# Kernel optimization log

Measured on AMD Instinct MI355X. Metric: run time of the kernel, lower is better.

Reference implementation:

```python
import jax, jax.numpy as jnp
import numpy as np

N = 50000      # nodes
E = 400000     # edges
IN_DIM = 128
HID = 64
HEADS1 = 4
OUT_DIM = 64
NEG_SLOPE = 0.2


def _gat_layer(x, W, attn_l, attn_r, bias, src, dst, heads, out_feats):
    # x: [N, F_in]; W: [F_in, heads*out]; attn_l/attn_r: [heads, out]; bias: [heads*out]
    n = x.shape[0]
    feat = (x @ W).reshape(n, heads, out_feats)              # [N, H, D]
    el = jnp.sum(feat * attn_l, axis=-1)                     # [N, H]
    er = jnp.sum(feat * attn_r, axis=-1)                     # [N, H]
    e = jax.nn.leaky_relu(el[src] + er[dst], NEG_SLOPE)      # [E, H]
    # segment softmax over incoming edges per destination node
    emax = jax.ops.segment_max(e, dst, num_segments=n)       # [N, H]
    ex = jnp.exp(e - emax[dst])                              # [E, H]
    denom = jax.ops.segment_sum(ex, dst, num_segments=n)     # [N, H]
    alpha = ex / denom[dst]                                  # [E, H]
    msg = alpha[:, :, None] * feat[src]                      # [E, H, D]
    rst = jax.ops.segment_sum(msg, dst, num_segments=n)      # [N, H, D]
    return rst + bias.reshape(1, heads, out_feats)


def setup_inputs() -> dict:
    key = jax.random.key(0)
    ks = jax.random.split(key, 12)
    features = jax.random.normal(ks[0], (N, IN_DIM), dtype=jnp.float32)
    src = jax.random.randint(ks[1], (E,), 0, N, dtype=jnp.int32)
    dst = jax.random.randint(ks[2], (E,), 0, N, dtype=jnp.int32)
    s1 = 1.0 / np.sqrt(IN_DIM)
    s2 = 1.0 / np.sqrt(HEADS1 * HID)
    W1 = jax.random.normal(ks[3], (IN_DIM, HEADS1 * HID), dtype=jnp.float32) * s1
    attn_l1 = jax.random.normal(ks[4], (HEADS1, HID), dtype=jnp.float32) * 0.1
    attn_r1 = jax.random.normal(ks[5], (HEADS1, HID), dtype=jnp.float32) * 0.1
    b1 = jnp.zeros((HEADS1 * HID,), dtype=jnp.float32)
    W2 = jax.random.normal(ks[6], (HEADS1 * HID, OUT_DIM), dtype=jnp.float32) * s2
    attn_l2 = jax.random.normal(ks[7], (1, OUT_DIM), dtype=jnp.float32) * 0.1
    attn_r2 = jax.random.normal(ks[8], (1, OUT_DIM), dtype=jnp.float32) * 0.1
    b2 = jnp.zeros((OUT_DIM,), dtype=jnp.float32)
    return {"features": features, "src": src, "dst": dst,
            "W1": W1, "attn_l1": attn_l1, "attn_r1": attn_r1, "b1": b1,
            "W2": W2, "attn_l2": attn_l2, "attn_r2": attn_r2, "b2": b2}


def reference(features, src, dst, W1, attn_l1, attn_r1, b1, W2, attn_l2, attn_r2, b2):
    h = _gat_layer(features, W1, attn_l1, attn_r1, b1, src, dst, HEADS1, HID)  # [N, 4, 64]
    h = h.reshape(h.shape[0], -1)                                             # flatten heads
    h = _gat_layer(h, W2, attn_l2, attn_r2, b2, src, dst, 1, OUT_DIM)         # [N, 1, 64]
    return h
```

## Files before the change

### kernel.cpp

```cpp
#include <hip/hip_runtime.h>
#include <hip/hip_bf16.h>

#define N_NODES 50000
#define N_EDGES 400000
#define IN_DIM 128
#define HID 64
#define HEADS 4
#define L1_OUT (HEADS * HID)
#define OUT_DIM 64
#define NEG_SLOPE 0.2f
#define SCAN_B 256
#define DCHUNK 128
#define HIST_B 1563

typedef short bf16x8 __attribute__((ext_vector_type(8)));
typedef float f32x4 __attribute__((ext_vector_type(4)));

__device__ __forceinline__ float leaky(float x) { return x > 0.f ? x : NEG_SLOPE * x; }

__device__ __forceinline__ unsigned short bfh(float x) {
    unsigned u = __float_as_uint(x);
    return (unsigned short)((u + 0x7fffu + ((u >> 16) & 1u)) >> 16);
}
__device__ __forceinline__ float fb(unsigned short h) {
    return __uint_as_float(((unsigned)h) << 16);
}

__global__ void hist_wprep_kernel(const int* __restrict__ dst, int* __restrict__ cnt,
                                  const float* __restrict__ W1, const float* __restrict__ W2,
                                  unsigned short* __restrict__ W1fh, unsigned short* __restrict__ W1fl,
                                  unsigned short* __restrict__ W2fh, unsigned short* __restrict__ W2fl) {
    int bid = blockIdx.x;
    if (bid < HIST_B) {
        int e = bid * 256 + threadIdx.x;
        if (e < N_EDGES) atomicAdd(&cnt[dst[e]], 1);
        return;
    }
    int s = (bid - HIST_B) * 256 + threadIdx.x;
    if (s < 4096) {
        int lane = s & 63, ks = (s >> 6) & 3, ntile = s >> 8;
        int n = ntile * 16 + (lane & 15);
        int kb = ks * 32 + (lane >> 4) * 8;
#pragma unroll
        for (int j = 0; j < 8; ++j) {
            float w = W1[(kb + j) * L1_OUT + n];
            unsigned short h = bfh(w);
            W1fh[s * 8 + j] = h;
            W1fl[s * 8 + j] = bfh(w - fb(h));
        }
    } else if (s < 6144) {
        int s2 = s - 4096;
        int lane = s2 & 63, ks = (s2 >> 6) & 7, ntile = s2 >> 9;
        int n = ntile * 16 + (lane & 15);
        int kb = ks * 32 + (lane >> 4) * 8;
#pragma unroll
        for (int j = 0; j < 8; ++j) {
            float w = W2[(kb + j) * OUT_DIM + n];
            unsigned short h = bfh(w);
            W2fh[s2 * 8 + j] = h;
            W2fl[s2 * 8 + j] = bfh(w - fb(h));
        }
    }
}

__global__ void scanA_kernel(const int* __restrict__ cnt, int* __restrict__ texcl,
                             int* __restrict__ bsum) {
    __shared__ int sh[SCAN_B];
    int tid = threadIdx.x;
    int i = blockIdx.x * SCAN_B + tid;
    int v = (i < N_NODES) ? cnt[i] : 0;
    sh[tid] = v;
    __syncthreads();
    for (int off = 1; off < SCAN_B; off <<= 1) {
        int t = (tid >= off) ? sh[tid - off] : 0;
        __syncthreads();
        sh[tid] += t;
        __syncthreads();
    }
    if (i < N_NODES) texcl[i] = sh[tid] - v;
    if (tid == SCAN_B - 1) bsum[blockIdx.x] = sh[tid];
}

__global__ void scanB_kernel(const int* __restrict__ bsum, int* __restrict__ bexcl, int nb) {
    __shared__ int sh[SCAN_B];
    int tid = threadIdx.x;
    int v = (tid < nb) ? bsum[tid] : 0;
    sh[tid] = v;
    __syncthreads();
    for (int off = 1; off < SCAN_B; off <<= 1) {
        int t = (tid >= off) ? sh[tid - off] : 0;
        __syncthreads();
        sh[tid] += t;
        __syncthreads();
    }
    if (tid < nb) bexcl[tid] = sh[tid] - v;
}

__global__ void scanC_kernel(const int* __restrict__ texcl, const int* __restrict__ bexcl,
                             int* __restrict__ row) {
    int i = blockIdx.x * blockDim.x + threadIdx.x;
    if (i < N_NODES) row[i] = texcl[i] + bexcl[i >> 8];
    if (blockIdx.x == 0 && threadIdx.x == 0) row[N_NODES] = N_EDGES;
}

__global__ void fill_kernel(const int* __restrict__ src, const int* __restrict__ dst,
                            const int* __restrict__ row, int* __restrict__ fc,
                            int* __restrict__ perm_src) {
    int e = blockIdx.x * blockDim.x + threadIdx.x;
    if (e >= N_EDGES) return;
    int d = dst[e];
    int p = row[d] + atomicAdd(&fc[d], 1);
    perm_src[p] = src[e];
}

__global__ __launch_bounds__(512) void gemm1_kernel(const float* __restrict__ X,
                                                    const unsigned short* __restrict__ W1fh,
                                                    const unsigned short* __restrict__ W1fl,
                                                    const float* __restrict__ al1,
                                                    const float* __restrict__ ar1,
                                                    unsigned short* __restrict__ feat1b,
                                                    float* __restrict__ el1,
                                                    float* __restrict__ er1) {
    __shared__ unsigned short Ah[4 * 4 * 64 * 8];
    __shared__ unsigned short Al[4 * 4 * 64 * 8];
    int t = threadIdx.x;
    int m0 = blockIdx.x * 64;

    {
        int m = t >> 3;
        int k0 = (t & 7) * 16;
        int mfrag = m >> 4, mrow = m & 15;
        bool valid = (m0 + m) < N_NODES;
        const float4* xr = (const float4*)&X[(size_t)(m0 + m) * IN_DIM];
#pragma unroll
        for (int g = 0; g < 4; ++g) {
            int k = k0 + g * 4;
            float4 v = valid ? xr[k >> 2] : float4{0.f, 0.f, 0.f, 0.f};
            int kstep = k >> 5, kk = k & 31;
            int lane = mrow + 16 * (kk >> 3);
            int j0 = kk & 7;
            int base = ((mfrag * 4 + kstep) * 64 + lane) * 8 + j0;
            unsigned short h0 = bfh(v.x), h1 = bfh(v.y), h2 = bfh(v.z), h3 = bfh(v.w);
            *(ushort4*)&Ah[base] = make_ushort4(h0, h1, h2, h3);
            *(ushort4*)&Al[base] = make_ushort4(bfh(v.x - fb(h0)), bfh(v.y - fb(h1)),
                                                bfh(v.z - fb(h2)), bfh(v.w - fb(h3)));
        }
    }
    __syncthreads();

    int w = t >> 6, lane = t & 63;
    int wr = w >> 2, wc = w & 3;
    f32x4 acc[2][4];
#pragma unroll
    for (int mi = 0; mi < 2; ++mi)
#pragma unroll
        for (int nf = 0; nf < 4; ++nf) acc[mi][nf] = f32x4{0.f, 0.f, 0.f, 0.f};

#pragma unroll
    for (int kstep = 0; kstep < 4; ++kstep) {
        bf16x8 a_h[2], a_l[2];
#pragma unroll
        for (int mi = 0; mi < 2; ++mi) {
            int slot = (((wr * 2 + mi) * 4 + kstep) * 64 + lane) * 8;
            a_h[mi] = *(const bf16x8*)&Ah[slot];
            a_l[mi] = *(const bf16x8*)&Al[slot];
        }
#pragma unroll
        for (int nf = 0; nf < 4; ++nf) {
            int slot = (((wc * 4 + nf) * 4 + kstep) * 64 + lane) * 8;
            bf16x8 b_h = *(const bf16x8*)&W1fh[slot];
            bf16x8 b_l = *(const bf16x8*)&W1fl[slot];
#pragma unroll
            for (int mi = 0; mi < 2; ++mi) {
                acc[mi][nf] = __builtin_amdgcn_mfma_f32_16x16x32_bf16(a_h[mi], b_h, acc[mi][nf], 0, 0, 0);
                acc[mi][nf] = __builtin_amdgcn_mfma_f32_16x16x32_bf16(a_h[mi], b_l, acc[mi][nf], 0, 0, 0);
                acc[mi][nf] = __builtin_amdgcn_mfma_f32_16x16x32_bf16(a_l[mi], b_h, acc[mi][nf], 0, 0, 0);
            }
        }
    }

    int fq = lane >> 4, fr = lane & 15;
#pragma unroll
    for (int mi = 0; mi < 2; ++mi) {
#pragma unroll
        for (int j = 0; j < 4; ++j) {
            int r = m0 + wr * 32 + mi * 16 + fq * 4 + j;
            if (r >= N_NODES) continue;
#pragma unroll
            for (int nf = 0; nf < 4; ++nf) {
                int c = wc * 64 + nf * 16 + fr;
                feat1b[(size_t)r * L1_OUT + c] = bfh(acc[mi][nf][j]);
            }
        }
    }

    float al_v[4], ar_v[4];
#pragma unroll
    for (int nf = 0; nf < 4; ++nf) {
        al_v[nf] = al1[wc * 64 + nf * 16 + fr];
        ar_v[nf] = ar1[wc * 64 + nf * 16 + fr];
    }
#pragma unroll
    for (int mi = 0; mi < 2; ++mi) {
#pragma unroll
        for (int j = 0; j < 4; ++j) {
            float l = 0.f, r = 0.f;
#pragma unroll
            for (int nf = 0; nf < 4; ++nf) {
                l += acc[mi][nf][j] * al_v[nf];
                r += acc[mi][nf][j] * ar_v[nf];
            }
#pragma unroll
            for (int off = 1; off < 16; off <<= 1) {
                l += __shfl_xor(l, off, 64);
                r += __shfl_xor(r, off, 64);
            }
            int rr = m0 + wr * 32 + mi * 16 + fq * 4 + j;
            if (fr == 0 && rr < N_NODES) {
                el1[rr * HEADS + wc] = l;
                er1[rr * HEADS + wc] = r;
            }
        }
    }
}

__global__ __launch_bounds__(256) void gather1_kernel(const int* __restrict__ row,
                                                      const int* __restrict__ perm_src,
                                                      const float* __restrict__ el1,
                                                      const float* __restrict__ er1,
                                                      const unsigned short* __restrict__ feat1b,
                                                      float* __restrict__ rst1) {
    __shared__ int psrc[4 * DCHUNK];
    __shared__ float alds[4 * DCHUNK * 4];
    int tid = threadIdx.x;
    int w = tid >> 6, lane = tid & 63;
    int d = blockIdx.x * 4 + w;
    int base = row[d], deg = row[d + 1] - base;
    bool fast = (deg > 0) && (deg <= DCHUNK);

    if (fast) {
        for (int j = lane; j < deg; j += 64) psrc[w * DCHUNK + j] = perm_src[base + j];
        int h = lane >> 4, jj = lane & 15;
        float er_d = er1[d * HEADS + h];
        float m = -1e30f;
        for (int j0 = 0; j0 < deg; j0 += 16) {
            int j = j0 + jj;
            if (j < deg) {
                float s = leaky(el1[psrc[w * DCHUNK + j] * HEADS + h] + er_d);
                alds[(w * DCHUNK + j) * 4 + h] = s;
                m = fmaxf(m, s);
            }
        }
#pragma unroll
        for (int off = 1; off < 16; off <<= 1) m = fmaxf(m, __shfl_xor(m, off, 64));
        float ss = 0.f;
        for (int j0 = 0; j0 < deg; j0 += 16) {
            int j = j0 + jj;
            if (j < deg) {
                float e = __expf(alds[(w * DCHUNK + j) * 4 + h] - m);
                alds[(w * DCHUNK + j) * 4 + h] = e;
                ss += e;
            }
        }
#pragma unroll
        for (int off = 1; off < 16; off <<= 1) ss += __shfl_xor(ss, off, 64);
        float inv = 1.f / ss;
        for (int j0 = 0; j0 < deg; j0 += 16) {
            int j = j0 + jj;
            if (j < deg) alds[(w * DCHUNK + j) * 4 + h] *= inv;
        }
    }
    __syncthreads();

    float4* out4 = (float4*)&rst1[(size_t)d * L1_OUT];
    if (deg == 0) {
        out4[lane] = float4{0.f, 0.f, 0.f, 0.f};
    } else if (fast) {
        int hh = lane >> 4;
        const ushort4* f4 = (const ushort4*)feat1b;
        float4 a0 = {0.f, 0.f, 0.f, 0.f}, a1 = {0.f, 0.f, 0.f, 0.f};
        float4 a2 = {0.f, 0.f, 0.f, 0.f}, a3 = {0.f, 0.f, 0.f, 0.f};
        int j = 0;
        for (; j + 3 < deg; j += 4) {
            int s0 = psrc[w * DCHUNK + j], s1 = psrc[w * DCHUNK + j + 1];
            int s2 = psrc[w * DCHUNK + j + 2], s3 = psrc[w * DCHUNK + j + 3];
            float w0 = alds[(w * DCHUNK + j) * 4 + hh], w1 = alds[(w * DCHUNK + j + 1) * 4 + hh];
            float w2 = alds[(w * DCHUNK + j + 2) * 4 + hh], w3 = alds[(w * DCHUNK + j + 3) * 4 + hh];
            ushort4 f0 = f4[(size_t)s0 * 64 + lane];
            ushort4 f1 = f4[(size_t)s1 * 64 + lane];
            ushort4 f2 = f4[(size_t)s2 * 64 + lane];
            ushort4 f3 = f4[(size_t)s3 * 64 + lane];
            a0.x += w0 * fb(f0.x); a0.y += w0 * fb(f0.y); a0.z += w0 * fb(f0.z); a0.w += w0 * fb(f0.w);
            a1.x += w1 * fb(f1.x); a1.y += w1 * fb(f1.y); a1.z += w1 * fb(f1.z); a1.w += w1 * fb(f1.w);
            a2.x += w2 * fb(f2.x); a2.y += w2 * fb(f2.y); a2.z += w2 * fb(f2.z); a2.w += w2 * fb(f2.w);
            a3.x += w3 * fb(f3.x); a3.y += w3 * fb(f3.y); a3.z += w3 * fb(f3.z); a3.w += w3 * fb(f3.w);
        }
        for (; j < deg; ++j) {
            int s0 = psrc[w * DCHUNK + j];
            float w0 = alds[(w * DCHUNK + j) * 4 + hh];
            ushort4 f0 = f4[(size_t)s0 * 64 + lane];
            a0.x += w0 * fb(f0.x); a0.y += w0 * fb(f0.y); a0.z += w0 * fb(f0.z); a0.w += w0 * fb(f0.w);
        }
        float4 r;
        r.x = a0.x + a1.x + a2.x + a3.x;
        r.y = a0.y + a1.y + a2.y + a3.y;
        r.z = a0.z + a1.z + a2.z + a3.z;
        r.w = a0.w + a1.w + a2.w + a3.w;
        out4[lane] = r;
    } else {
        float mh0, mh1, mh2, mh3, iv0, iv1, iv2, iv3;
#pragma unroll
        for (int h = 0; h < 4; ++h) {
            float er_dh = er1[d * HEADS + h];
            float m = -1e30f;
            for (int j = lane; j < deg; j += 64)
                m = fmaxf(m, leaky(el1[perm_src[base + j] * HEADS + h] + er_dh));
#pragma unroll
            for (int off = 1; off < 64; off <<= 1) m = fmaxf(m, __shfl_xor(m, off, 64));
            float ss = 0.f;
            for (int j = lane; j < deg; j += 64)
                ss += __expf(leaky(el1[perm_src[base + j] * HEADS + h] + er_dh) - m);
#pragma unroll
            for (int off = 1; off < 64; off <<= 1) ss += __shfl_xor(ss, off, 64);
            float iv = 1.f / ss;
            if (h == 0) { mh0 = m; iv0 = iv; }
            else if (h == 1) { mh1 = m; iv1 = iv; }
            else if (h == 2) { mh2 = m; iv2 = iv; }
            else { mh3 = m; iv3 = iv; }
        }
        int hh = lane >> 4;
        float m_s = hh == 0 ? mh0 : hh == 1 ? mh1 : hh == 2 ? mh2 : mh3;
        float iv_s = hh == 0 ? iv0 : hh == 1 ? iv1 : hh == 2 ? iv2 : iv3;
        float er_s = er1[d * HEADS + hh];
        const ushort4* f4 = (const ushort4*)feat1b;
        float4 a0 = {0.f, 0.f, 0.f, 0.f};
        for (int j = 0; j < deg; ++j) {
            int s = perm_src[base + j];
            float a = __expf(leaky(el1[s * HEADS + hh] + er_s) - m_s) * iv_s;
            ushort4 f0 = f4[(size_t)s * 64 + lane];
            a0.x += a * fb(f0.x); a0.y += a * fb(f0.y); a0.z += a * fb(f0.z); a0.w += a * fb(f0.w);
        }
        out4[lane] = a0;
    }
}

__global__ __launch_bounds__(256) void gemm2_kernel(const float* __restrict__ rst1,
                                                    const float* __restrict__ b1,
                                                    const unsigned short* __restrict__ W2fh,
                                                    const unsigned short* __restrict__ W2fl,
                                                    const float* __restrict__ al2,
                                                    const float* __restrict__ ar2,
                                                    unsigned short* __restrict__ feat2b,
                                                    float* __restrict__ el2,
                                                    float* __restrict__ er2) {
    __shared__ unsigned short Ah[2 * 8 * 64 * 8];
    __shared__ unsigned short Al[2 * 8 * 64 * 8];
    __shared__ float pl[2][2][16], pr[2][2][16];
    int t = threadIdx.x;
    int n0 = blockIdx.x * 32;

    {
        int m = t >> 3;
        int kstep = t & 7;
        int mfrag = m >> 4, mrow = m & 15;
        bool valid = (n0 + m) < N_NODES;
        const float4* ar4 = (const float4*)&rst1[(size_t)(n0 + m) * L1_OUT];
        const float4* br4 = (const float4*)b1;
#pragma unroll
        for (int g = 0; g < 8; ++g) {
            int k = kstep * 32 + g * 4;
            float4 v = valid ? ar4[k >> 2] : float4{0.f, 0.f, 0.f, 0.f};
            float4 bb = br4[k >> 2];
            v.x += bb.x; v.y += bb.y; v.z += bb.z; v.w += bb.w;
            if (!valid) { v.x = 0.f; v.y = 0.f; v.z = 0.f; v.w = 0.f; }
            int lane = mrow + 16 * (g >> 1);
            int j0 = (g & 1) * 4;
            int base = ((mfrag * 8 + kstep) * 64 + lane) * 8 + j0;
            unsigned short h0 = bfh(v.x), h1 = bfh(v.y), h2 = bfh(v.z), h3 = bfh(v.w);
            *(ushort4*)&Ah[base] = make_ushort4(h0, h1, h2, h3);
            *(ushort4*)&Al[base] = make_ushort4(bfh(v.x - fb(h0)), bfh(v.y - fb(h1)),
                                                bfh(v.z - fb(h2)), bfh(v.w - fb(h3)));
        }
    }
    __syncthreads();

    int w = t >> 6, lane = t & 63;
    int mi = w >> 1, nh = w & 1;
    f32x4 acc[2];
    acc[0] = f32x4{0.f, 0.f, 0.f, 0.f};
    acc[1] = f32x4{0.f, 0.f, 0.f, 0.f};

#pragma unroll
    for (int ks = 0; ks < 8; ++ks) {
        int aslot = ((mi * 8 + ks) * 64 + lane) * 8;
        bf16x8 a_h = *(const bf16x8*)&Ah[aslot];
        bf16x8 a_l = *(const bf16x8*)&Al[aslot];
#pragma unroll
        for (int nf = 0; nf < 2; ++nf) {
            int ntile = nh * 2 + nf;
            int slot = ((ntile * 8 + ks) * 64 + lane) * 8;
            bf16x8 b_h = *(const bf16x8*)&W2fh[slot];
            bf16x8 b_l = *(const bf16x8*)&W2fl[slot];
            acc[nf] = __builtin_amdgcn_mfma_f32_16x16x32_bf16(a_h, b_h, acc[nf], 0, 0, 0);
            acc[nf] = __builtin_amdgcn_mfma_f32_16x16x32_bf16(a_h, b_l, acc[nf], 0, 0, 0);
            acc[nf] = __builtin_amdgcn_mfma_f32_16x16x32_bf16(a_l, b_h, acc[nf], 0, 0, 0);
        }
    }

    int fq = lane >> 4, fr = lane & 15;
#pragma unroll
    for (int j = 0; j < 4; ++j) {
        int r = n0 + mi * 16 + fq * 4 + j;
        if (r >= N_NODES) continue;
#pragma unroll
        for (int nf = 0; nf < 2; ++nf) {
            int c = (nh * 2 + nf) * 16 + fr;
            feat2b[(size_t)r * OUT_DIM + c] = bfh(acc[nf][j]);
        }
    }

    float al_v[2], ar_v[2];
#pragma unroll
    for (int nf = 0; nf < 2; ++nf) {
        al_v[nf] = al2[(nh * 2 + nf) * 16 + fr];
        ar_v[nf] = ar2[(nh * 2 + nf) * 16 + fr];
    }
#pragma unroll
    for (int j = 0; j < 4; ++j) {
        float l = acc[0][j] * al_v[0] + acc[1][j] * al_v[1];
        float r = acc[0][j] * ar_v[0] + acc[1][j] * ar_v[1];
#pragma unroll
        for (int off = 1; off < 16; off <<= 1) {
            l += __shfl_xor(l, off, 64);
            r += __shfl_xor(r, off, 64);
        }
        if (fr == 0) {
            pl[nh][mi][fq * 4 + j] = l;
            pr[nh][mi][fq * 4 + j] = r;
        }
    }
    __syncthreads();
    if (t < 32) {
        int n = n0 + t;
        if (n < N_NODES) {
            int mi2 = t >> 4, rr = t & 15;
            el2[n] = pl[0][mi2][rr] + pl[1][mi2][rr];
            er2[n] = pr[0][mi2][rr] + pr[1][mi2][rr];
        }
    }
}

__global__ __launch_bounds__(256) void gather2_kernel(const int* __restrict__ row,
                                                      const int* __restrict__ perm_src,
                                                      const float* __restrict__ el2,
                                                      const float* __restrict__ er2,
                                                      const unsigned short* __restrict__ feat2b,
                                                      const float* __restrict__ b2,
                                                      float* __restrict__ out) {
    __shared__ int psrc[4 * DCHUNK];
    __shared__ float alds[4 * DCHUNK];
    int tid = threadIdx.x;
    int w = tid >> 6, lane = tid & 63;
    int d = blockIdx.x * 4 + w;
    int base = row[d], deg = row[d + 1] - base;
    bool fast = (deg > 0) && (deg <= DCHUNK);

    if (fast) {
        for (int j = lane; j < deg; j += 64) psrc[w * DCHUNK + j] = perm_src[base + j];
        float er_d = er2[d];
        float m = -1e30f;
        for (int j0 = 0; j0 < deg; j0 += 64) {
            int j = j0 + lane;
            if (j < deg) {
                float s = leaky(el2[psrc[w * DCHUNK + j]] + er_d);
                alds[w * DCHUNK + j] = s;
                m = fmaxf(m, s);
            }
        }
#pragma unroll
        for (int off = 1; off < 64; off <<= 1) m = fmaxf(m, __shfl_xor(m, off, 64));
        float ss = 0.f;
        for (int j0 = 0; j0 < deg; j0 += 64) {
            int j = j0 + lane;
            if (j < deg) {
                float e = __expf(alds[w * DCHUNK + j] - m);
                alds[w * DCHUNK + j] = e;
                ss += e;
            }
        }
#pragma unroll
        for (int off = 1; off < 64; off <<= 1) ss += __shfl_xor(ss, off, 64);
        float inv = 1.f / ss;
        for (int j0 = 0; j0 < deg; j0 += 64) {
            int j = j0 + lane;
            if (j < deg) alds[w * DCHUNK + j] *= inv;
        }
    }
    __syncthreads();

    if (deg == 0) {
        out[(size_t)d * OUT_DIM + lane] = b2[lane];
    } else if (fast) {
        float a0 = 0.f, a1 = 0.f, a2 = 0.f, a3 = 0.f;
        int j = 0;
        for (; j + 3 < deg; j += 4) {
            int s0 = psrc[w * DCHUNK + j], s1 = psrc[w * DCHUNK + j + 1];
            int s2 = psrc[w * DCHUNK + j + 2], s3 = psrc[w * DCHUNK + j + 3];
            float w0 = alds[w * DCHUNK + j], w1 = alds[w * DCHUNK + j + 1];
            float w2 = alds[w * DCHUNK + j + 2], w3 = alds[w * DCHUNK + j + 3];
            a0 += w0 * fb(feat2b[(size_t)s0 * OUT_DIM + lane]);
            a1 += w1 * fb(feat2b[(size_t)s1 * OUT_DIM + lane]);
            a2 += w2 * fb(feat2b[(size_t)s2 * OUT_DIM + lane]);
            a3 += w3 * fb(feat2b[(size_t)s3 * OUT_DIM + lane]);
        }
        for (; j < deg; ++j) {
            a0 += alds[w * DCHUNK + j] * fb(feat2b[(size_t)psrc[w * DCHUNK + j] * OUT_DIM + lane]);
        }
        out[(size_t)d * OUT_DIM + lane] = a0 + a1 + a2 + a3 + b2[lane];
    } else {
        float er_d = er2[d];
        float m = -1e30f;
        for (int j = lane; j < deg; j += 64)
            m = fmaxf(m, leaky(el2[perm_src[base + j]] + er_d));
#pragma unroll
        for (int off = 1; off < 64; off <<= 1) m = fmaxf(m, __shfl_xor(m, off, 64));
        float ss = 0.f;
        for (int j = lane; j < deg; j += 64)
            ss += __expf(leaky(el2[perm_src[base + j]] + er_d) - m);
#pragma unroll
        for (int off = 1; off < 64; off <<= 1) ss += __shfl_xor(ss, off, 64);
        float inv = 1.f / ss;
        float a0 = 0.f;
        for (int j = 0; j < deg; ++j) {
            int s = perm_src[base + j];
            float a = __expf(leaky(el2[s] + er_d) - m) * inv;
            a0 += a * fb(feat2b[(size_t)s * OUT_DIM + lane]);
        }
        out[(size_t)d * OUT_DIM + lane] = a0 + b2[lane];
    }
}

extern "C" void kernel_launch(void* const* d_in, const int* in_sizes, int n_in,
                              void* d_out, int out_size, void* d_ws, size_t ws_size,
                              hipStream_t stream) {
    const float* features = (const float*)d_in[0];
    const int* src = (const int*)d_in[1];
    const int* dst = (const int*)d_in[2];
    const float* W1 = (const float*)d_in[3];
    const float* al1 = (const float*)d_in[4];
    const float* ar1 = (const float*)d_in[5];
    const float* b1 = (const float*)d_in[6];
    const float* W2 = (const float*)d_in[7];
    const float* al2 = (const float*)d_in[8];
    const float* ar2 = (const float*)d_in[9];
    const float* b2 = (const float*)d_in[10];
    float* out = (float*)d_out;

    float* ws = (float*)d_ws;
    float* rst1 = ws;
    float* el1 = rst1 + (size_t)N_NODES * L1_OUT;
    float* er1 = el1 + N_NODES * HEADS;
    float* el2 = er1 + N_NODES * HEADS;
    float* er2 = el2 + N_NODES;
    unsigned short* feat1b = (unsigned short*)(er2 + N_NODES);
    unsigned short* feat2b = feat1b + (size_t)N_NODES * L1_OUT;
    unsigned short* W1fh = feat2b + (size_t)N_NODES * OUT_DIM;
    unsigned short* W1fl = W1fh + 32768;
    unsigned short* W2fh = W1fl + 32768;
    unsigned short* W2fl = W2fh + 16384;
    int* cnt = (int*)(W2fl + 16384);
    int* fc = cnt + N_NODES;
    int* texcl = fc + N_NODES;
    int* bsum = texcl + N_NODES;
    int* bexcl = bsum + 256;
    int* row = bexcl + 256;
    int* perm_src = row + N_NODES + 1;

    const int nscan = (N_NODES + SCAN_B - 1) / SCAN_B;

    hipMemsetAsync(cnt, 0, (size_t)2 * N_NODES * sizeof(int), stream);

    hist_wprep_kernel<<<HIST_B + 24, 256, 0, stream>>>(dst, cnt, W1, W2, W1fh, W1fl, W2fh, W2fl);
    scanA_kernel<<<nscan, SCAN_B, 0, stream>>>(cnt, texcl, bsum);
    scanB_kernel<<<1, SCAN_B, 0, stream>>>(bsum, bexcl, nscan);
    scanC_kernel<<<(N_NODES + 255) / 256, 256, 0, stream>>>(texcl, bexcl, row);
    fill_kernel<<<(N_EDGES + 255) / 256, 256, 0, stream>>>(src, dst, row, fc, perm_src);

    gemm1_kernel<<<(N_NODES + 63) / 64, 512, 0, stream>>>(features, W1fh, W1fl, al1, ar1,
                                                          feat1b, el1, er1);
    gather1_kernel<<<N_NODES / 4, 256, 0, stream>>>(row, perm_src, el1, er1, feat1b, rst1);

    gemm2_kernel<<<(N_NODES + 31) / 32, 256, 0, stream>>>(rst1, b1, W2fh, W2fl, al2, ar2,
                                                          feat2b, el2, er2);
    gather2_kernel<<<N_NODES / 4, 256, 0, stream>>>(row, perm_src, el2, er2, feat2b, b2, out);
}
```

Before: 193.9 us.

## Fuse layer-1 aggregation into layer-2 GEMM and use register shuffles for softmax

Merges the layer-1 gather/softmax aggregation into the layer-2 GEMM kernel. Each block aggregates its 32 destination rows straight into the split-bf16 LDS tiles, so the fp32 rst1 intermediate (N×256) is never written to or read back from global memory, and one launch is removed. The low-degree softmax paths in both gathers now keep source indices and alpha in registers and broadcast them with shuffles instead of staging them in LDS. The trade-off is a lower fast-path degree threshold (16 for layer 1, 64 for layer 2). The fused kernel also processes 8 rows per wave serially, with fewer blocks and less parallelism for hiding latency.

```diff
diff --git a/kernel.cpp b/kernel.cpp
--- a/kernel.cpp
+++ b/kernel.cpp
@@ -10,7 +10,6 @@
 #define OUT_DIM 64
 #define NEG_SLOPE 0.2f
 #define SCAN_B 256
-#define DCHUNK 128
 #define HIST_B 1563
 
 typedef short bf16x8 __attribute__((ext_vector_type(8)));
@@ -224,171 +223,134 @@
     }
 }
 
-__global__ __launch_bounds__(256) void gather1_kernel(const int* __restrict__ row,
-                                                      const int* __restrict__ perm_src,
-                                                      const float* __restrict__ el1,
-                                                      const float* __restrict__ er1,
-                                                      const unsigned short* __restrict__ feat1b,
-                                                      float* __restrict__ rst1) {
-    __shared__ int psrc[4 * DCHUNK];
-    __shared__ float alds[4 * DCHUNK * 4];
-    int tid = threadIdx.x;
-    int w = tid >> 6, lane = tid & 63;
-    int d = blockIdx.x * 4 + w;
-    int base = row[d], deg = row[d + 1] - base;
-    bool fast = (deg > 0) && (deg <= DCHUNK);
-
-    if (fast) {
-        for (int j = lane; j < deg; j += 64) psrc[w * DCHUNK + j] = perm_src[base + j];
-        int h = lane >> 4, jj = lane & 15;
-        float er_d = er1[d * HEADS + h];
-        float m = -1e30f;
-        for (int j0 = 0; j0 < deg; j0 += 16) {
-            int j = j0 + jj;
-            if (j < deg) {
-                float s = leaky(el1[psrc[w * DCHUNK + j] * HEADS + h] + er_d);
-                alds[(w * DCHUNK + j) * 4 + h] = s;
-                m = fmaxf(m, s);
-            }
-        }
-#pragma unroll
-        for (int off = 1; off < 16; off <<= 1) m = fmaxf(m, __shfl_xor(m, off, 64));
-        float ss = 0.f;
-        for (int j0 = 0; j0 < deg; j0 += 16) {
-            int j = j0 + jj;
-            if (j < deg) {
-                float e = __expf(alds[(w * DCHUNK + j) * 4 + h] - m);
-                alds[(w * DCHUNK + j) * 4 + h] = e;
-                ss += e;
-            }
-        }
-#pragma unroll
-        for (int off = 1; off < 16; off <<= 1) ss += __shfl_xor(ss, off, 64);
-        float inv = 1.f / ss;
-        for (int j0 = 0; j0 < deg; j0 += 16) {
-            int j = j0 + jj;
-            if (j < deg) alds[(w * DCHUNK + j) * 4 + h] *= inv;
-        }
-    }
-    __syncthreads();
-
-    float4* out4 = (float4*)&rst1[(size_t)d * L1_OUT];
-    if (deg == 0) {
-        out4[lane] = float4{0.f, 0.f, 0.f, 0.f};
-    } else if (fast) {
-        int hh = lane >> 4;
-        const ushort4* f4 = (const ushort4*)feat1b;
-        float4 a0 = {0.f, 0.f, 0.f, 0.f}, a1 = {0.f, 0.f, 0.f, 0.f};
-        float4 a2 = {0.f, 0.f, 0.f, 0.f}, a3 = {0.f, 0.f, 0.f, 0.f};
-        int j = 0;
-        for (; j + 3 < deg; j += 4) {
-            int s0 = psrc[w * DCHUNK + j], s1 = psrc[w * DCHUNK + j + 1];
-            int s2 = psrc[w * DCHUNK + j + 2], s3 = psrc[w * DCHUNK + j + 3];
-            float w0 = alds[(w * DCHUNK + j) * 4 + hh], w1 = alds[(w * DCHUNK + j + 1) * 4 + hh];
-            float w2 = alds[(w * DCHUNK + j + 2) * 4 + hh], w3 = alds[(w * DCHUNK + j + 3) * 4 + hh];
-            ushort4 f0 = f4[(size_t)s0 * 64 + lane];
-            ushort4 f1 = f4[(size_t)s1 * 64 + lane];
-            ushort4 f2 = f4[(size_t)s2 * 64 + lane];
-            ushort4 f3 = f4[(size_t)s3 * 64 + lane];
-            a0.x += w0 * fb(f0.x); a0.y += w0 * fb(f0.y); a0.z += w0 * fb(f0.z); a0.w += w0 * fb(f0.w);
-            a1.x += w1 * fb(f1.x); a1.y += w1 * fb(f1.y); a1.z += w1 * fb(f1.z); a1.w += w1 * fb(f1.w);
-            a2.x += w2 * fb(f2.x); a2.y += w2 * fb(f2.y); a2.z += w2 * fb(f2.z); a2.w += w2 * fb(f2.w);
-            a3.x += w3 * fb(f3.x); a3.y += w3 * fb(f3.y); a3.z += w3 * fb(f3.z); a3.w += w3 * fb(f3.w);
-        }
-        for (; j < deg; ++j) {
-            int s0 = psrc[w * DCHUNK + j];
-            float w0 = alds[(w * DCHUNK + j) * 4 + hh];
-            ushort4 f0 = f4[(size_t)s0 * 64 + lane];
-            a0.x += w0 * fb(f0.x); a0.y += w0 * fb(f0.y); a0.z += w0 * fb(f0.z); a0.w += w0 * fb(f0.w);
-        }
-        float4 r;
-        r.x = a0.x + a1.x + a2.x + a3.x;
-        r.y = a0.y + a1.y + a2.y + a3.y;
-        r.z = a0.z + a1.z + a2.z + a3.z;
-        r.w = a0.w + a1.w + a2.w + a3.w;
-        out4[lane] = r;
-    } else {
-        float mh0, mh1, mh2, mh3, iv0, iv1, iv2, iv3;
-#pragma unroll
-        for (int h = 0; h < 4; ++h) {
-            float er_dh = er1[d * HEADS + h];
-            float m = -1e30f;
-            for (int j = lane; j < deg; j += 64)
-                m = fmaxf(m, leaky(el1[perm_src[base + j] * HEADS + h] + er_dh));
-#pragma unroll
-            for (int off = 1; off < 64; off <<= 1) m = fmaxf(m, __shfl_xor(m, off, 64));
-            float ss = 0.f;
-            for (int j = lane; j < deg; j += 64)
-                ss += __expf(leaky(el1[perm_src[base + j] * HEADS + h] + er_dh) - m);
-#pragma unroll
-            for (int off = 1; off < 64; off <<= 1) ss += __shfl_xor(ss, off, 64);
-            float iv = 1.f / ss;
-            if (h == 0) { mh0 = m; iv0 = iv; }
-            else if (h == 1) { mh1 = m; iv1 = iv; }
-            else if (h == 2) { mh2 = m; iv2 = iv; }
-            else { mh3 = m; iv3 = iv; }
-        }
-        int hh = lane >> 4;
-        float m_s = hh == 0 ? mh0 : hh == 1 ? mh1 : hh == 2 ? mh2 : mh3;
-        float iv_s = hh == 0 ? iv0 : hh == 1 ? iv1 : hh == 2 ? iv2 : iv3;
-        float er_s = er1[d * HEADS + hh];
-        const ushort4* f4 = (const ushort4*)feat1b;
-        float4 a0 = {0.f, 0.f, 0.f, 0.f};
-        for (int j = 0; j < deg; ++j) {
-            int s = perm_src[base + j];
-            float a = __expf(leaky(el1[s * HEADS + hh] + er_s) - m_s) * iv_s;
-            ushort4 f0 = f4[(size_t)s * 64 + lane];
-            a0.x += a * fb(f0.x); a0.y += a * fb(f0.y); a0.z += a * fb(f0.z); a0.w += a * fb(f0.w);
-        }
-        out4[lane] = a0;
-    }
-}
-
-__global__ __launch_bounds__(256) void gemm2_kernel(const float* __restrict__ rst1,
-                                                    const float* __restrict__ b1,
-                                                    const unsigned short* __restrict__ W2fh,
-                                                    const unsigned short* __restrict__ W2fl,
-                                                    const float* __restrict__ al2,
-                                                    const float* __restrict__ ar2,
-                                                    unsigned short* __restrict__ feat2b,
-                                                    float* __restrict__ el2,
-                                                    float* __restrict__ er2) {
+__global__ __launch_bounds__(256) void layer2_kernel(const int* __restrict__ row,
+                                                     const int* __restrict__ perm_src,
+                                                     const float* __restrict__ el1,
+                                                     const float* __restrict__ er1,
+                                                     const unsigned short* __restrict__ feat1b,
+                                                     const float* __restrict__ b1,
+                                                     const unsigned short* __restrict__ W2fh,
+                                                     const unsigned short* __restrict__ W2fl,
+                                                     const float* __restrict__ al2,
+                                                     const float* __restrict__ ar2,
+                                                     unsigned short* __restrict__ feat2b,
+                                                     float* __restrict__ el2,
+                                                     float* __restrict__ er2) {
     __shared__ unsigned short Ah[2 * 8 * 64 * 8];
     __shared__ unsigned short Al[2 * 8 * 64 * 8];
     __shared__ float pl[2][2][16], pr[2][2][16];
     int t = threadIdx.x;
+    int w = t >> 6, lane = t & 63;
     int n0 = blockIdx.x * 32;
 
-    {
-        int m = t >> 3;
-        int kstep = t & 7;
+    float4 b1v = *(const float4*)&b1[lane * 4];
+    const ushort4* f4 = (const ushort4*)feat1b;
+
+#pragma unroll 1
+    for (int it = 0; it < 8; ++it) {
+        int d = n0 + it * 4 + w;
+        float4 acc = {0.f, 0.f, 0.f, 0.f};
+        bool valid = d < N_NODES;
+        if (valid) {
+            int base = row[d], deg = row[d + 1] - base;
+            if (deg > 0 && deg <= 16) {
+                int h = lane >> 4, jj = lane & 15;
+                int s_reg = (jj < deg) ? perm_src[base + jj] : 0;
+                float er_d = er1[d * HEADS + h];
+                float sc = (jj < deg) ? leaky(el1[s_reg * HEADS + h] + er_d) : -1e30f;
+                float m = sc;
+                m = fmaxf(m, __shfl_xor(m, 1, 64));
+                m = fmaxf(m, __shfl_xor(m, 2, 64));
+                m = fmaxf(m, __shfl_xor(m, 4, 64));
+                m = fmaxf(m, __shfl_xor(m, 8, 64));
+                float ex = (jj < deg) ? __expf(sc - m) : 0.f;
+                float ss = ex;
+                ss += __shfl_xor(ss, 1, 64);
+                ss += __shfl_xor(ss, 2, 64);
+                ss += __shfl_xor(ss, 4, 64);
+                ss += __shfl_xor(ss, 8, 64);
+                float alpha = ex / ss;
+                int hb = lane & 48;
+                float4 A0 = {0.f,0.f,0.f,0.f}, A1 = {0.f,0.f,0.f,0.f};
+                float4 A2 = {0.f,0.f,0.f,0.f}, A3 = {0.f,0.f,0.f,0.f};
+                int j = 0;
+                for (; j + 3 < deg; j += 4) {
+                    int s0 = __shfl(s_reg, j), s1 = __shfl(s_reg, j + 1);
+                    int s2 = __shfl(s_reg, j + 2), s3 = __shfl(s_reg, j + 3);
+                    float a0 = __shfl(alpha, hb + j), a1 = __shfl(alpha, hb + j + 1);
+                    float a2 = __shfl(alpha, hb + j + 2), a3 = __shfl(alpha, hb + j + 3);
+                    ushort4 f0 = f4[(size_t)s0 * 64 + lane];
+                    ushort4 f1 = f4[(size_t)s1 * 64 + lane];
+                    ushort4 f2 = f4[(size_t)s2 * 64 + lane];
+                    ushort4 f3 = f4[(size_t)s3 * 64 + lane];
+                    A0.x += a0 * fb(f0.x); A0.y += a0 * fb(f0.y); A0.z += a0 * fb(f0.z); A0.w += a0 * fb(f0.w);
+                    A1.x += a1 * fb(f1.x); A1.y += a1 * fb(f1.y); A1.z += a1 * fb(f1.z); A1.w += a1 * fb(f1.w);
+                    A2.x += a2 * fb(f2.x); A2.y += a2 * fb(f2.y); A2.z += a2 * fb(f2.z); A2.w += a2 * fb(f2.w);
+                    A3.x += a3 * fb(f3.x); A3.y += a3 * fb(f3.y); A3.z += a3 * fb(f3.z); A3.w += a3 * fb(f3.w);
+                }
+                for (; j < deg; ++j) {
+                    int s0 = __shfl(s_reg, j);
+                    float a0 = __shfl(alpha, hb + j);
+                    ushort4 f0 = f4[(size_t)s0 * 64 + lane];
+                    A0.x += a0 * fb(f0.x); A0.y += a0 * fb(f0.y); A0.z += a0 * fb(f0.z); A0.w += a0 * fb(f0.w);
+                }
+                acc.x = A0.x + A1.x + A2.x + A3.x;
+                acc.y = A0.y + A1.y + A2.y + A3.y;
+                acc.z = A0.z + A1.z + A2.z + A3.z;
+                acc.w = A0.w + A1.w + A2.w + A3.w;
+            } else if (deg > 16) {
+                float mh0, mh1, mh2, mh3, iv0, iv1, iv2, iv3;
+#pragma unroll
+                for (int h = 0; h < 4; ++h) {
+                    float er_dh = er1[d * HEADS + h];
+                    float m = -1e30f;
+                    for (int j = lane; j < deg; j += 64)
+                        m = fmaxf(m, leaky(el1[perm_src[base + j] * HEADS + h] + er_dh));
+#pragma unroll
+                    for (int off = 1; off < 64; off <<= 1) m = fmaxf(m, __shfl_xor(m, off, 64));
+                    float ss = 0.f;
+                    for (int j = lane; j < deg; j += 64)
+                        ss += __expf(leaky(el1[perm_src[base + j] * HEADS + h] + er_dh) - m);
+#pragma unroll
+                    for (int off = 1; off < 64; off <<= 1) ss += __shfl_xor(ss, off, 64);
+                    float iv = 1.f / ss;
+                    if (h == 0) { mh0 = m; iv0 = iv; }
+                    else if (h == 1) { mh1 = m; iv1 = iv; }
+                    else if (h == 2) { mh2 = m; iv2 = iv; }
+                    else { mh3 = m; iv3 = iv; }
+                }
+                int hh = lane >> 4;
+                float m_s = hh == 0 ? mh0 : hh == 1 ? mh1 : hh == 2 ? mh2 : mh3;
+                float iv_s = hh == 0 ? iv0 : hh == 1 ? iv1 : hh == 2 ? iv2 : iv3;
+                float er_s = er1[d * HEADS + hh];
+                for (int j = 0; j < deg; ++j) {
+                    int s = perm_src[base + j];
+                    float a = __expf(leaky(el1[s * HEADS + hh] + er_s) - m_s) * iv_s;
+                    ushort4 f0 = f4[(size_t)s * 64 + lane];
+                    acc.x += a * fb(f0.x); acc.y += a * fb(f0.y);
+                    acc.z += a * fb(f0.z); acc.w += a * fb(f0.w);
+                }
+            }
+            acc.x += b1v.x; acc.y += b1v.y; acc.z += b1v.z; acc.w += b1v.w;
+        }
+        int m = it * 4 + w;
         int mfrag = m >> 4, mrow = m & 15;
-        bool valid = (n0 + m) < N_NODES;
-        const float4* ar4 = (const float4*)&rst1[(size_t)(n0 + m) * L1_OUT];
-        const float4* br4 = (const float4*)b1;
-#pragma unroll
-        for (int g = 0; g < 8; ++g) {
-            int k = kstep * 32 + g * 4;
-            float4 v = valid ? ar4[k >> 2] : float4{0.f, 0.f, 0.f, 0.f};
-            float4 bb = br4[k >> 2];
-            v.x += bb.x; v.y += bb.y; v.z += bb.z; v.w += bb.w;
-            if (!valid) { v.x = 0.f; v.y = 0.f; v.z = 0.f; v.w = 0.f; }
-            int lane = mrow + 16 * (g >> 1);
-            int j0 = (g & 1) * 4;
-            int base = ((mfrag * 8 + kstep) * 64 + lane) * 8 + j0;
-            unsigned short h0 = bfh(v.x), h1 = bfh(v.y), h2 = bfh(v.z), h3 = bfh(v.w);
-            *(ushort4*)&Ah[base] = make_ushort4(h0, h1, h2, h3);
-            *(ushort4*)&Al[base] = make_ushort4(bfh(v.x - fb(h0)), bfh(v.y - fb(h1)),
-                                                bfh(v.z - fb(h2)), bfh(v.w - fb(h3)));
-        }
+        int c = lane * 4;
+        int kstep = c >> 5;
+        int fraglane = mrow + 16 * ((c & 31) >> 3);
+        int j0 = c & 7;
+        int basei = ((mfrag * 8 + kstep) * 64 + fraglane) * 8 + j0;
+        unsigned short h0 = bfh(acc.x), h1 = bfh(acc.y), h2 = bfh(acc.z), h3 = bfh(acc.w);
+        *(ushort4*)&Ah[basei] = make_ushort4(h0, h1, h2, h3);
+        *(ushort4*)&Al[basei] = make_ushort4(bfh(acc.x - fb(h0)), bfh(acc.y - fb(h1)),
+                                             bfh(acc.z - fb(h2)), bfh(acc.w - fb(h3)));
     }
     __syncthreads();
 
-    int w = t >> 6, lane = t & 63;
     int mi = w >> 1, nh = w & 1;
-    f32x4 acc[2];
-    acc[0] = f32x4{0.f, 0.f, 0.f, 0.f};
-    acc[1] = f32x4{0.f, 0.f, 0.f, 0.f};
+    f32x4 acc2[2];
+    acc2[0] = f32x4{0.f, 0.f, 0.f, 0.f};
+    acc2[1] = f32x4{0.f, 0.f, 0.f, 0.f};
 
 #pragma unroll
     for (int ks = 0; ks < 8; ++ks) {
@@ -401,9 +363,9 @@
             int slot = ((ntile * 8 + ks) * 64 + lane) * 8;
             bf16x8 b_h = *(const bf16x8*)&W2fh[slot];
             bf16x8 b_l = *(const bf16x8*)&W2fl[slot];
-            acc[nf] = __builtin_amdgcn_mfma_f32_16x16x32_bf16(a_h, b_h, acc[nf], 0, 0, 0);
-            acc[nf] = __builtin_amdgcn_mfma_f32_16x16x32_bf16(a_h, b_l, acc[nf], 0, 0, 0);
-            acc[nf] = __builtin_amdgcn_mfma_f32_16x16x32_bf16(a_l, b_h, acc[nf], 0, 0, 0);
+            acc2[nf] = __builtin_amdgcn_mfma_f32_16x16x32_bf16(a_h, b_h, acc2[nf], 0, 0, 0);
+            acc2[nf] = __builtin_amdgcn_mfma_f32_16x16x32_bf16(a_h, b_l, acc2[nf], 0, 0, 0);
+            acc2[nf] = __builtin_amdgcn_mfma_f32_16x16x32_bf16(a_l, b_h, acc2[nf], 0, 0, 0);
         }
     }
 
@@ -415,7 +377,7 @@
 #pragma unroll
         for (int nf = 0; nf < 2; ++nf) {
             int c = (nh * 2 + nf) * 16 + fr;
-            feat2b[(size_t)r * OUT_DIM + c] = bfh(acc[nf][j]);
+            feat2b[(size_t)r * OUT_DIM + c] = bfh(acc2[nf][j]);
         }
     }
 
@@ -427,8 +389,8 @@
     }
 #pragma unroll
     for (int j = 0; j < 4; ++j) {
-        float l = acc[0][j] * al_v[0] + acc[1][j] * al_v[1];
-        float r = acc[0][j] * ar_v[0] + acc[1][j] * ar_v[1];
+        float l = acc2[0][j] * al_v[0] + acc2[1][j] * al_v[1];
+        float r = acc2[0][j] * ar_v[0] + acc2[1][j] * ar_v[1];
 #pragma unroll
         for (int off = 1; off < 16; off <<= 1) {
             l += __shfl_xor(l, off, 64);
@@ -457,66 +419,45 @@
                                                       const unsigned short* __restrict__ feat2b,
                                                       const float* __restrict__ b2,
                                                       float* __restrict__ out) {
-    __shared__ int psrc[4 * DCHUNK];
-    __shared__ float alds[4 * DCHUNK];
     int tid = threadIdx.x;
     int w = tid >> 6, lane = tid & 63;
     int d = blockIdx.x * 4 + w;
     int base = row[d], deg = row[d + 1] - base;
-    bool fast = (deg > 0) && (deg <= DCHUNK);
-
-    if (fast) {
-        for (int j = lane; j < deg; j += 64) psrc[w * DCHUNK + j] = perm_src[base + j];
+    float bias = b2[lane];
+    if (deg == 0) {
+        out[(size_t)d * OUT_DIM + lane] = bias;
+        return;
+    }
+    if (deg <= 64) {
+        int s_reg = (lane < deg) ? perm_src[base + lane] : 0;
         float er_d = er2[d];
-        float m = -1e30f;
-        for (int j0 = 0; j0 < deg; j0 += 64) {
-            int j = j0 + lane;
-            if (j < deg) {
-                float s = leaky(el2[psrc[w * DCHUNK + j]] + er_d);
-                alds[w * DCHUNK + j] = s;
-                m = fmaxf(m, s);
-            }
-        }
+        float sc = (lane < deg) ? leaky(el2[s_reg] + er_d) : -1e30f;
+        float m = sc;
 #pragma unroll
         for (int off = 1; off < 64; off <<= 1) m = fmaxf(m, __shfl_xor(m, off, 64));
-        float ss = 0.f;
-        for (int j0 = 0; j0 < deg; j0 += 64) {
-            int j = j0 + lane;
-            if (j < deg) {
-                float e = __expf(alds[w * DCHUNK + j] - m);
-                alds[w * DCHUNK + j] = e;
-                ss += e;
-            }
-        }
+        float ex = (lane < deg) ? __expf(sc - m) : 0.f;
+        float ss = ex;
 #pragma unroll
         for (int off = 1; off < 64; off <<= 1) ss += __shfl_xor(ss, off, 64);
-        float inv = 1.f / ss;
-        for (int j0 = 0; j0 < deg; j0 += 64) {
-            int j = j0 + lane;
-            if (j < deg) alds[w * DCHUNK + j] *= inv;
-        }
-    }
-    __syncthreads();
-
-    if (deg == 0) {
-        out[(size_t)d * OUT_DIM + lane] = b2[lane];
-    } else if (fast) {
+        float alpha = ex / ss;
         float a0 = 0.f, a1 = 0.f, a2 = 0.f, a3 = 0.f;
         int j = 0;
         for (; j + 3 < deg; j += 4) {
-            int s0 = psrc[w * DCHUNK + j], s1 = psrc[w * DCHUNK + j + 1];
-            int s2 = psrc[w * DCHUNK + j + 2], s3 = psrc[w * DCHUNK + j + 3];
-            float w0 = alds[w * DCHUNK + j], w1 = alds[w * DCHUNK + j + 1];
-            float w2 = alds[w * DCHUNK + j + 2], w3 = alds[w * DCHUNK + j + 3];
+            int s0 = __shfl(s_reg, j), s1 = __shfl(s_reg, j + 1);
+            int s2 = __shfl(s_reg, j + 2), s3 = __shfl(s_reg, j + 3);
+            float w0 = __shfl(alpha, j), w1 = __shfl(alpha, j + 1);
+            float w2 = __shfl(alpha, j + 2), w3 = __shfl(alpha, j + 3);
             a0 += w0 * fb(feat2b[(size_t)s0 * OUT_DIM + lane]);
             a1 += w1 * fb(feat2b[(size_t)s1 * OUT_DIM + lane]);
             a2 += w2 * fb(feat2b[(size_t)s2 * OUT_DIM + lane]);
             a3 += w3 * fb(feat2b[(size_t)s3 * OUT_DIM + lane]);
         }
         for (; j < deg; ++j) {
-            a0 += alds[w * DCHUNK + j] * fb(feat2b[(size_t)psrc[w * DCHUNK + j] * OUT_DIM + lane]);
-        }
-        out[(size_t)d * OUT_DIM + lane] = a0 + a1 + a2 + a3 + b2[lane];
+            int s0 = __shfl(s_reg, j);
+            float w0 = __shfl(alpha, j);
+            a0 += w0 * fb(feat2b[(size_t)s0 * OUT_DIM + lane]);
+        }
+        out[(size_t)d * OUT_DIM + lane] = a0 + a1 + a2 + a3 + bias;
     } else {
         float er_d = er2[d];
         float m = -1e30f;
@@ -536,7 +477,7 @@
             float a = __expf(leaky(el2[s] + er_d) - m) * inv;
             a0 += a * fb(feat2b[(size_t)s * OUT_DIM + lane]);
         }
-        out[(size_t)d * OUT_DIM + lane] = a0 + b2[lane];
+        out[(size_t)d * OUT_DIM + lane] = a0 + bias;
     }
 }
 
@@ -557,8 +498,7 @@
     float* out = (float*)d_out;
 
     float* ws = (float*)d_ws;
-    float* rst1 = ws;
-    float* el1 = rst1 + (size_t)N_NODES * L1_OUT;
+    float* el1 = ws;
     float* er1 = el1 + N_NODES * HEADS;
     float* el2 = er1 + N_NODES * HEADS;
     float* er2 = el2 + N_NODES;
@@ -588,9 +528,8 @@
 
     gemm1_kernel<<<(N_NODES + 63) / 64, 512, 0, stream>>>(features, W1fh, W1fl, al1, ar1,
                                                           feat1b, el1, er1);
-    gather1_kernel<<<N_NODES / 4, 256, 0, stream>>>(row, perm_src, el1, er1, feat1b, rst1);
-
-    gemm2_kernel<<<(N_NODES + 31) / 32, 256, 0, stream>>>(rst1, b1, W2fh, W2fl, al2, ar2,
-                                                          feat2b, el2, er2);
+    layer2_kernel<<<(N_NODES + 31) / 32, 256, 0, stream>>>(row, perm_src, el1, er1, feat1b,
+                                                           b1, W2fh, W2fl, al2, ar2,
+                                                           feat2b, el2, er2);
     gather2_kernel<<<N_NODES / 4, 256, 0, stream>>>(row, perm_src, el2, er2, feat2b, b2, out);
 }
```

Measured after the change: 181.7 us. 6.3% less time.
